# Kernel tuning notes

Measured on AMD Instinct MI355X. Metric: run time of the kernel, lower is better.

Reference implementation:

```python
import jax, jax.numpy as jnp
import numpy as np

H = 128          # num_hidden
B, L, K, M = 4, 2048, 24, 64   # batch, residues, neighbors-per-residue, ligand atoms
FF = 4 * H       # feed-forward width
EPS = 1e-5       # LayerNorm eps (torch default)


def _gelu(x):
    return jax.nn.gelu(x, approximate=False)  # torch nn.GELU default (erf)


def _ln(x, s, b):
    mu = jnp.mean(x, axis=-1, keepdims=True)
    var = jnp.mean(jnp.square(x - mu), axis=-1, keepdims=True)
    return (x - mu) * jax.lax.rsqrt(var + EPS) * s + b


def _lin(x, w, b):
    return x @ w.T + b


def setup_inputs() -> dict:
    key = jax.random.key(0)
    ks = iter(jax.random.split(key, 40))
    # uniqueness makes the reference deterministic and equal to scatter-add.
    nn_idx = jnp.argsort(jax.random.uniform(next(ks), (B, L, M)), axis=-1)[:, :, :K].astype(jnp.int32)
    inp = {
        "nn_idx": nn_idx,
        "Y_scale": jax.random.uniform(next(ks), (B, M), jnp.float32, 1.0, 30.0),
        "h_Y_nodes": jax.random.normal(next(ks), (B, L, K, H), jnp.float32),
        "h_E_context": jax.random.normal(next(ks), (B, L, K, H), jnp.float32),
        "h_V": jax.random.normal(next(ks), (B, L, H), jnp.float32),
    }
    def lin_params(fan_in, fan_out):
        w = jax.random.normal(next(ks), (fan_out, fan_in), jnp.float32) / np.sqrt(fan_in).astype(np.float32)
        b = jnp.zeros((fan_out,), jnp.float32)
        return w, b
    for name, fi, fo in [("W1", 3 * H, H), ("W2", H, H), ("W3", H, H),
                         ("W11", 3 * H, H), ("W12", H, H), ("W13", H, H),
                         ("Win", H, FF), ("Wout", FF, H)]:
        inp[name + "_w"], inp[name + "_b"] = lin_params(fi, fo)
    for name in ("n1", "n2", "n3"):
        inp[name + "_s"] = jnp.ones((H,), jnp.float32)
        inp[name + "_b"] = jnp.zeros((H,), jnp.float32)
    return inp


def reference(nn_idx, Y_scale, h_Y_nodes, h_E_context, h_V,
              W1_w, W1_b, W2_w, W2_b, W3_w, W3_b,
              W11_w, W11_b, W12_w, W12_b, W13_w, W13_b,
              Win_w, Win_b, Wout_w, Wout_b,
              n1_s, n1_b, n2_s, n2_b, n3_s, n3_b):
    h_V_exp = jnp.broadcast_to(h_V[:, :, None, :], (B, L, K, H))
    h_YEV = jnp.concatenate([h_Y_nodes, h_E_context, h_V_exp], axis=-1)  # [B,L,K,3H]
    msg = _lin(_gelu(_lin(_gelu(_lin(h_YEV, W1_w, W1_b)), W2_w, W2_b)), W3_w, W3_b)
    # scatter per (b,l) with unique idx, then sum over l == segment-sum over (b, atom)
    seg_ids = (jnp.arange(B, dtype=jnp.int32)[:, None, None] * M + nn_idx).reshape(-1)
    dh = jax.ops.segment_sum(msg.reshape(-1, H), seg_ids, num_segments=B * M).reshape(B, M, H)
    dh = dh / Y_scale[:, :, None]
    # gather_context_atom_features: dh[b, nn_idx[b,l,k]]
    dh = jnp.take_along_axis(dh, nn_idx.reshape(B, L * K)[:, :, None], axis=1).reshape(B, L, K, H)
    h_Y = _ln(h_Y_nodes + dh, n1_s, n1_b)
    h_Y = _ln(h_Y + _lin(_gelu(_lin(h_Y, Win_w, Win_b)), Wout_w, Wout_b), n2_s, n2_b)
    h_YEV = jnp.concatenate([h_Y, h_E_context, h_V_exp], axis=-1)
    msg = _lin(_gelu(_lin(_gelu(_lin(h_YEV, W11_w, W11_b)), W12_w, W12_b)), W13_w, W13_b)
    h_E = _ln(h_E_context + msg, n3_s, n3_b)
    return (h_Y, h_E)
```

## Files before the change

### kernel.cpp

```cpp
#include <hip/hip_runtime.h>
#include <hip/hip_bf16.h>

#define H_   128
#define B_   4
#define L_   2048
#define KN   24
#define M_   64
#define NROW (B_*L_*KN)
#define LKR  (L_*KN)

typedef float f32x4 __attribute__((ext_vector_type(4)));
typedef short s16x8 __attribute__((ext_vector_type(8)));

#define MFMA16(a,b,c) __builtin_amdgcn_mfma_f32_16x16x32_bf16((a),(b),(c),0,0,0)

static __device__ __forceinline__ unsigned short f2bfu(float x){
    union { __hip_bfloat16 h; unsigned short s; } u; u.h = __float2bfloat16(x); return u.s;
}
static __device__ __forceinline__ float bf2f(unsigned short s){
    union { unsigned short s; __hip_bfloat16 h; } u; u.s = s; return __bfloat162float(u.h);
}
static __device__ __forceinline__ unsigned packbf(float lo, float hi){
    return (unsigned)f2bfu(lo) | ((unsigned)f2bfu(hi) << 16);
}
static __device__ __forceinline__ float gelu_f(float x){
    const float x2 = x*x;
    const float u  = x * fmaf(x2, -0.10294265f, -2.3022083f);
    const float e  = __builtin_amdgcn_exp2f(u);
    return x * __builtin_amdgcn_rcpf(1.0f + e);
}
static __device__ __forceinline__ float wsum(float v){
#pragma unroll
    for (int m = 32; m; m >>= 1) v += __shfl_xor(v, m, 64);
    return v;
}
static __device__ __forceinline__ s16x8 cvt8(float4 p0, float4 p1){
    s16x8 v;
    v[0]=(short)f2bfu(p0.x); v[1]=(short)f2bfu(p0.y); v[2]=(short)f2bfu(p0.z); v[3]=(short)f2bfu(p0.w);
    v[4]=(short)f2bfu(p1.x); v[5]=(short)f2bfu(p1.y); v[6]=(short)f2bfu(p1.z); v[7]=(short)f2bfu(p1.w);
    return v;
}
template<int KW>
static __device__ __forceinline__ s16x8 afrag(const short* xs, int r, int blk){
    return *(const s16x8*)(xs + r*KW + ((blk ^ (r & 7)) << 3));
}
template<int KW>
static __device__ __forceinline__ void bstore(short* xs, int r, int c, unsigned v){
    *(unsigned*)(xs + r*KW + ((((c >> 3) ^ (r & 7))) << 3) + (c & 7)) = v;
}
static __device__ __forceinline__ int fidx(int r, int c){
    return r*128 + ((((c >> 2) ^ (r & 7))) << 2) + (c & 3);
}

template<int KWACT, int NKS>
static __device__ __forceinline__ void mm_sw(const short* act, const short* __restrict__ Wp,
    int ktS, int kt0, int tn0, int lane, f32x4 (&acc)[2][2])
{
    const int cl = lane & 15, rq = lane >> 4;
    const s16x8* W8 = (const s16x8*)Wp;
#pragma unroll
    for (int ks = 0; ks < NKS; ++ks){
        const int blk = (ks << 2) + rq;
        const s16x8 a0 = afrag<KWACT>(act, cl, blk);
        const s16x8 a1 = afrag<KWACT>(act, 16 + cl, blk);
#pragma unroll
        for (int t = 0; t < 2; ++t){
            const s16x8 wf = W8[(size_t)((tn0 + t)*ktS + kt0 + ks)*64 + lane];
            acc[0][t] = MFMA16(wf, a0, acc[0][t]);
            acc[1][t] = MFMA16(wf, a1, acc[1][t]);
        }
    }
}
template<int KWACT, int NKS>
static __device__ __forceinline__ void mm_nat(const short* act, const short* __restrict__ Wp,
    int ktS, int kt0, int tn0, int lane, f32x4 (&acc)[2][2])
{
    const int cl = lane & 15, rq = lane >> 4;
    const s16x8* W8 = (const s16x8*)Wp;
#pragma unroll
    for (int ks = 0; ks < NKS; ++ks){
        const int blk = (ks << 2) + rq;
        const s16x8 a0 = afrag<KWACT>(act, cl, blk);
        const s16x8 a1 = afrag<KWACT>(act, 16 + cl, blk);
#pragma unroll
        for (int t = 0; t < 2; ++t){
            const s16x8 wf = W8[(size_t)((tn0 + t)*ktS + kt0 + ks)*64 + lane];
            acc[0][t] = MFMA16(a0, wf, acc[0][t]);
            acc[1][t] = MFMA16(a1, wf, acc[1][t]);
        }
    }
}

struct PackArgs {
    const float* src[8];
    int K[8];
    int off[8];
};
#define PACK_TOTAL 294912
__global__ void k_pack(PackArgs pa, short* __restrict__ dst){
    const int gid = blockIdx.x*256 + threadIdx.x;
    if (gid >= PACK_TOTAL) return;
    int w = 0;
#pragma unroll
    for (int i = 1; i < 8; ++i) if (gid >= pa.off[i]) w = i;
    const int e = gid - pa.off[w];
    const int K = pa.K[w];
    const int j = e & 7, lane = (e >> 3) & 63, tt = e >> 9;
    const int kt = K >> 5;
    const int tk = tt % kt, tn = tt / kt;
    const int row = tn*16 + (lane & 15);
    const int col = tk*32 + ((lane >> 4) << 3) + j;
    dst[gid] = (short)f2bfu(pa.src[w][(size_t)row*K + col]);
}

__global__ void k_zero(float* __restrict__ dh){
    const int i = blockIdx.x*256 + threadIdx.x;
    if (i < B_*M_*H_) dh[i] = 0.0f;
}
__global__ void k_scale(float* __restrict__ dh, const float* __restrict__ Ys){
    const int i = blockIdx.x*256 + threadIdx.x;
    if (i < B_*M_*H_) dh[i] = dh[i] / Ys[i >> 7];
}

__global__ __launch_bounds__(256) void k_msg(
    const float* __restrict__ hY, const float* __restrict__ hE, const float* __restrict__ hV,
    const int* __restrict__ nn,
    const short* __restrict__ W1p, const float* __restrict__ B1,
    const short* __restrict__ W2p, const float* __restrict__ B2,
    const short* __restrict__ W3p, const float* __restrict__ B3,
    float* __restrict__ dh)
{
    __shared__ short xs[32*384];
    __shared__ short tb1[32*128];
    __shared__ short tb2[32*128];
    const int tid = threadIdx.x, lane = tid & 63, w = tid >> 6;
    const int cl = lane & 15, rq = lane >> 4;
    const int row0 = blockIdx.x * 32, b = row0 / LKR;
    const int tn0 = 2*w;

    for (int c = tid; c < 32*48; c += 256){
        const int rr = c/48, k = (c - rr*48) << 3, g = row0 + rr;
        const float* s = (k < 128) ? hY + (size_t)g*128 + k
                      : (k < 256) ? hE + (size_t)g*128 + (k-128)
                                  : hV + (size_t)(g/KN)*128 + (k-256);
        float4 p0 = ((const float4*)s)[0], p1 = ((const float4*)s)[1];
        *(s16x8*)(xs + rr*384 + ((((k>>3) ^ (rr&7))) << 3)) = cvt8(p0, p1);
    }
    __syncthreads();

    f32x4 acc[2][2];
#pragma unroll
    for (int t = 0; t < 2; ++t)
#pragma unroll
        for (int j = 0; j < 4; ++j){
            const float bv = B1[(tn0+t)*16 + rq*4 + j];
            acc[0][t][j] = bv; acc[1][t][j] = bv;
        }
    mm_sw<384,12>(xs, W1p, 12, 0, tn0, lane, acc);
#pragma unroll
    for (int rt = 0; rt < 2; ++rt)
#pragma unroll
        for (int t = 0; t < 2; ++t){
            const int r = rt*16 + cl, cb = (tn0+t)*16 + rq*4;
            bstore<128>(tb1, r, cb,   packbf(gelu_f(acc[rt][t][0]), gelu_f(acc[rt][t][1])));
            bstore<128>(tb1, r, cb+2, packbf(gelu_f(acc[rt][t][2]), gelu_f(acc[rt][t][3])));
        }
    __syncthreads();

#pragma unroll
    for (int t = 0; t < 2; ++t)
#pragma unroll
        for (int j = 0; j < 4; ++j){
            const float bv = B2[(tn0+t)*16 + rq*4 + j];
            acc[0][t][j] = bv; acc[1][t][j] = bv;
        }
    mm_sw<128,4>(tb1, W2p, 4, 0, tn0, lane, acc);
#pragma unroll
    for (int rt = 0; rt < 2; ++rt)
#pragma unroll
        for (int t = 0; t < 2; ++t){
            const int r = rt*16 + cl, cb = (tn0+t)*16 + rq*4;
            bstore<128>(tb2, r, cb,   packbf(gelu_f(acc[rt][t][0]), gelu_f(acc[rt][t][1])));
            bstore<128>(tb2, r, cb+2, packbf(gelu_f(acc[rt][t][2]), gelu_f(acc[rt][t][3])));
        }
    __syncthreads();

    f32x4 a3[2][2];
#pragma unroll
    for (int t = 0; t < 2; ++t){
        const float bv = B3[(tn0+t)*16 + cl];
        a3[0][t] = (f32x4){bv,bv,bv,bv};
        a3[1][t] = (f32x4){bv,bv,bv,bv};
    }
    mm_nat<128,4>(tb2, W3p, 4, 0, tn0, lane, a3);

#pragma unroll
    for (int rt = 0; rt < 2; ++rt){
        int mj[4];
#pragma unroll
        for (int j = 0; j < 4; ++j) mj[j] = nn[row0 + rt*16 + rq*4 + j];
#pragma unroll
        for (int t = 0; t < 2; ++t){
            const int c = (tn0+t)*16 + cl;
#pragma unroll
            for (int j = 0; j < 4; ++j)
                __hip_atomic_fetch_add(dh + ((size_t)(b*M_ + mj[j]))*128 + c, a3[rt][t][j],
                                       __ATOMIC_RELAXED, __HIP_MEMORY_SCOPE_AGENT);
        }
    }
}

__global__ __launch_bounds__(256) void k_hy(
    const float* __restrict__ hY, const float* __restrict__ dhs, const int* __restrict__ nn,
    const short* __restrict__ Winp, const float* __restrict__ Bin,
    const short* __restrict__ Woutp, const float* __restrict__ Bout,
    const float* __restrict__ n1s, const float* __restrict__ n1b,
    const float* __restrict__ n2s, const float* __restrict__ n2b,
    float* __restrict__ outY)
{
    __shared__ float tf[32*128];
    __shared__ short xb[32*128];
    __shared__ short ffc[32*128];
    const int tid = threadIdx.x, lane = tid & 63, w = tid >> 6;
    const int cl = lane & 15, rq = lane >> 4;
    const int row0 = blockIdx.x * 32, b = row0 / LKR;

    for (int c = tid; c < 32*16; c += 256){
        const int rr = c >> 4, k = (c & 15) << 3, g = row0 + rr;
        const int m = nn[g];
        const float* a = hY  + (size_t)g*128 + k;
        const float* d = dhs + ((size_t)(b*M_ + m))*128 + k;
        float4 a0 = ((const float4*)a)[0], a1 = ((const float4*)a)[1];
        float4 d0 = ((const float4*)d)[0], d1 = ((const float4*)d)[1];
        float4 r0 = {a0.x+d0.x, a0.y+d0.y, a0.z+d0.z, a0.w+d0.w};
        float4 r1 = {a1.x+d1.x, a1.y+d1.y, a1.z+d1.z, a1.w+d1.w};
        const int s = rr & 7, kb = k >> 2;
        *(float4*)&tf[rr*128 + ((kb ^ s) << 2)]     = r0;
        *(float4*)&tf[rr*128 + (((kb+1) ^ s) << 2)] = r1;
    }
    __syncthreads();

#pragma unroll
    for (int i = 0; i < 8; ++i){
        const int r = w*8 + i;
        const float v0 = tf[fidx(r, lane)], v1 = tf[fidx(r, lane+64)];
        const float mu = wsum(v0+v1) * (1.0f/128.0f);
        const float d0 = v0-mu, d1 = v1-mu;
        const float var = wsum(d0*d0 + d1*d1) * (1.0f/128.0f);
        const float rs = rsqrtf(var + 1e-5f);
        const float y0 = d0*rs*n1s[lane]    + n1b[lane];
        const float y1 = d1*rs*n1s[lane+64] + n1b[lane+64];
        const int c1 = lane + 64;
        xb[r*128 + ((((lane>>3) ^ (r&7))) << 3) + (lane&7)] = (short)f2bfu(y0);
        xb[r*128 + ((((c1>>3)   ^ (r&7))) << 3) + (c1&7)]   = (short)f2bfu(y1);
    }
    __syncthreads();

    f32x4 accW[2][2];
#pragma unroll
    for (int t = 0; t < 2; ++t)
#pragma unroll
        for (int j = 0; j < 4; ++j){
            const float bv = Bout[(2*w+t)*16 + rq*4 + j];
            accW[0][t][j] = bv; accW[1][t][j] = bv;
        }

    for (int p = 0; p < 4; ++p){
        f32x4 ai[2][2];
#pragma unroll
        for (int t = 0; t < 2; ++t)
#pragma unroll
            for (int j = 0; j < 4; ++j){
                const float bv = Bin[p*128 + (2*w+t)*16 + rq*4 + j];
                ai[0][t][j] = bv; ai[1][t][j] = bv;
            }
        mm_sw<128,4>(xb, Winp, 4, 0, p*8 + 2*w, lane, ai);
        __syncthreads();
#pragma unroll
        for (int rt = 0; rt < 2; ++rt)
#pragma unroll
            for (int t = 0; t < 2; ++t){
                const int r = rt*16 + cl, cb = (2*w+t)*16 + rq*4;
                bstore<128>(ffc, r, cb,   packbf(gelu_f(ai[rt][t][0]), gelu_f(ai[rt][t][1])));
                bstore<128>(ffc, r, cb+2, packbf(gelu_f(ai[rt][t][2]), gelu_f(ai[rt][t][3])));
            }
        __syncthreads();
        mm_sw<128,4>(ffc, Woutp, 16, p*4, 2*w, lane, accW);
    }

#pragma unroll
    for (int rt = 0; rt < 2; ++rt)
#pragma unroll
        for (int t = 0; t < 2; ++t){
            const int r = rt*16 + cl, cb = (2*w+t)*16 + rq*4;
            float4 o = {accW[rt][t][0], accW[rt][t][1], accW[rt][t][2], accW[rt][t][3]};
            *(float4*)&tf[r*128 + ((((cb>>2) ^ (r&7))) << 2)] = o;
        }
    __syncthreads();

#pragma unroll
    for (int i = 0; i < 8; ++i){
        const int r = w*8 + i, g = row0 + r;
        const int c1 = lane + 64;
        const float x0 = bf2f((unsigned short)xb[r*128 + ((((lane>>3) ^ (r&7))) << 3) + (lane&7)]);
        const float x1 = bf2f((unsigned short)xb[r*128 + ((((c1>>3)   ^ (r&7))) << 3) + (c1&7)]);
        const float v0 = tf[fidx(r, lane)]    + x0;
        const float v1 = tf[fidx(r, lane+64)] + x1;
        const float mu = wsum(v0+v1) * (1.0f/128.0f);
        const float d0 = v0-mu, d1 = v1-mu;
        const float var = wsum(d0*d0 + d1*d1) * (1.0f/128.0f);
        const float rs = rsqrtf(var + 1e-5f);
        outY[(size_t)g*128 + lane]      = d0*rs*n2s[lane]    + n2b[lane];
        outY[(size_t)g*128 + lane + 64] = d1*rs*n2s[lane+64] + n2b[lane+64];
    }
}

__global__ __launch_bounds__(256) void k_he(
    const float* __restrict__ hYn, const float* __restrict__ hE, const float* __restrict__ hV,
    const short* __restrict__ W1p, const float* __restrict__ B1,
    const short* __restrict__ W2p, const float* __restrict__ B2,
    const short* __restrict__ W3p, const float* __restrict__ B3,
    const float* __restrict__ n3s, const float* __restrict__ n3b,
    float* __restrict__ outE)
{
    __shared__ __align__(16) char pool[40960];
    short* xs  = (short*)pool;
    float* tf  = (float*)pool;
    short* tb1 = (short*)(pool + 24576);
    short* tb2 = (short*)(pool + 32768);
    const int tid = threadIdx.x, lane = tid & 63, w = tid >> 6;
    const int cl = lane & 15, rq = lane >> 4;
    const int row0 = blockIdx.x * 32;
    const int tn0 = 2*w;

    for (int c = tid; c < 32*48; c += 256){
        const int rr = c/48, k = (c - rr*48) << 3, g = row0 + rr;
        const float* s = (k < 128) ? hYn + (size_t)g*128 + k
                      : (k < 256) ? hE  + (size_t)g*128 + (k-128)
                                  : hV  + (size_t)(g/KN)*128 + (k-256);
        float4 p0 = ((const float4*)s)[0], p1 = ((const float4*)s)[1];
        *(s16x8*)(xs + rr*384 + ((((k>>3) ^ (rr&7))) << 3)) = cvt8(p0, p1);
    }
    __syncthreads();

    f32x4 acc[2][2];
#pragma unroll
    for (int t = 0; t < 2; ++t)
#pragma unroll
        for (int j = 0; j < 4; ++j){
            const float bv = B1[(tn0+t)*16 + rq*4 + j];
            acc[0][t][j] = bv; acc[1][t][j] = bv;
        }
    mm_sw<384,12>(xs, W1p, 12, 0, tn0, lane, acc);
#pragma unroll
    for (int rt = 0; rt < 2; ++rt)
#pragma unroll
        for (int t = 0; t < 2; ++t){
            const int r = rt*16 + cl, cb = (tn0+t)*16 + rq*4;
            bstore<128>(tb1, r, cb,   packbf(gelu_f(acc[rt][t][0]), gelu_f(acc[rt][t][1])));
            bstore<128>(tb1, r, cb+2, packbf(gelu_f(acc[rt][t][2]), gelu_f(acc[rt][t][3])));
        }
    __syncthreads();

#pragma unroll
    for (int t = 0; t < 2; ++t)
#pragma unroll
        for (int j = 0; j < 4; ++j){
            const float bv = B2[(tn0+t)*16 + rq*4 + j];
            acc[0][t][j] = bv; acc[1][t][j] = bv;
        }
    mm_sw<128,4>(tb1, W2p, 4, 0, tn0, lane, acc);
#pragma unroll
    for (int rt = 0; rt < 2; ++rt)
#pragma unroll
        for (int t = 0; t < 2; ++t){
            const int r = rt*16 + cl, cb = (tn0+t)*16 + rq*4;
            bstore<128>(tb2, r, cb,   packbf(gelu_f(acc[rt][t][0]), gelu_f(acc[rt][t][1])));
            bstore<128>(tb2, r, cb+2, packbf(gelu_f(acc[rt][t][2]), gelu_f(acc[rt][t][3])));
        }
    __syncthreads();

#pragma unroll
    for (int t = 0; t < 2; ++t)
#pragma unroll
        for (int j = 0; j < 4; ++j){
            const float bv = B3[(tn0+t)*16 + rq*4 + j];
            acc[0][t][j] = bv; acc[1][t][j] = bv;
        }
    mm_sw<128,4>(tb2, W3p, 4, 0, tn0, lane, acc);

#pragma unroll
    for (int rt = 0; rt < 2; ++rt)
#pragma unroll
        for (int t = 0; t < 2; ++t){
            const int r = rt*16 + cl, cb = (tn0+t)*16 + rq*4;
            float4 o = {acc[rt][t][0], acc[rt][t][1], acc[rt][t][2], acc[rt][t][3]};
            *(float4*)&tf[r*128 + ((((cb>>2) ^ (r&7))) << 2)] = o;
        }
    __syncthreads();

#pragma unroll
    for (int i = 0; i < 8; ++i){
        const int r = w*8 + i, g = row0 + r;
        const float v0 = tf[fidx(r, lane)]    + hE[(size_t)g*128 + lane];
        const float v1 = tf[fidx(r, lane+64)] + hE[(size_t)g*128 + lane + 64];
        const float mu = wsum(v0+v1) * (1.0f/128.0f);
        const float d0 = v0-mu, d1 = v1-mu;
        const float var = wsum(d0*d0 + d1*d1) * (1.0f/128.0f);
        const float rs = rsqrtf(var + 1e-5f);
        outE[(size_t)g*128 + lane]      = d0*rs*n3s[lane]    + n3b[lane];
        outE[(size_t)g*128 + lane + 64] = d1*rs*n3s[lane+64] + n3b[lane+64];
    }
}

extern "C" void kernel_launch(void* const* d_in, const int* in_sizes, int n_in,
                              void* d_out, int out_size, void* d_ws, size_t ws_size,
                              hipStream_t stream) {
    const int*   nn   = (const int*)  d_in[0];
    const float* Ys   = (const float*)d_in[1];
    const float* hY   = (const float*)d_in[2];
    const float* hE   = (const float*)d_in[3];
    const float* hV   = (const float*)d_in[4];
    const float* W1w  = (const float*)d_in[5];  const float* W1b  = (const float*)d_in[6];
    const float* W2w  = (const float*)d_in[7];  const float* W2b  = (const float*)d_in[8];
    const float* W3w  = (const float*)d_in[9];  const float* W3b  = (const float*)d_in[10];
    const float* W11w = (const float*)d_in[11]; const float* W11b = (const float*)d_in[12];
    const float* W12w = (const float*)d_in[13]; const float* W12b = (const float*)d_in[14];
    const float* W13w = (const float*)d_in[15]; const float* W13b = (const float*)d_in[16];
    const float* Winw = (const float*)d_in[17]; const float* Winb = (const float*)d_in[18];
    const float* Woutw= (const float*)d_in[19]; const float* Woutb= (const float*)d_in[20];
    const float* n1s  = (const float*)d_in[21]; const float* n1b  = (const float*)d_in[22];
    const float* n2s  = (const float*)d_in[23]; const float* n2b  = (const float*)d_in[24];
    const float* n3s  = (const float*)d_in[25]; const float* n3b  = (const float*)d_in[26];

    float* outY = (float*)d_out;
    float* outE = outY + (size_t)NROW * H_;

    float* dh = (float*)d_ws;
    short* wp = (short*)((char*)d_ws + 131072);

    const int oW1 = 0,       oW2 = 49152,   oW3 = 65536,   oW11 = 81920;
    const int oW12 = 131072, oW13 = 147456, oWin = 163840, oWout = 229376;

    PackArgs pa;
    pa.src[0]=W1w;  pa.K[0]=384; pa.off[0]=oW1;
    pa.src[1]=W2w;  pa.K[1]=128; pa.off[1]=oW2;
    pa.src[2]=W3w;  pa.K[2]=128; pa.off[2]=oW3;
    pa.src[3]=W11w; pa.K[3]=384; pa.off[3]=oW11;
    pa.src[4]=W12w; pa.K[4]=128; pa.off[4]=oW12;
    pa.src[5]=W13w; pa.K[5]=128; pa.off[5]=oW13;
    pa.src[6]=Winw; pa.K[6]=128; pa.off[6]=oWin;
    pa.src[7]=Woutw;pa.K[7]=512; pa.off[7]=oWout;

    const int nblk = NROW / 32;

    k_pack <<<(PACK_TOTAL + 255)/256, 256, 0, stream>>>(pa, wp);
    k_zero <<<(B_*M_*H_ + 255)/256, 256, 0, stream>>>(dh);
    k_msg  <<<nblk, 256, 0, stream>>>(hY, hE, hV, nn,
                                      wp + oW1, W1b, wp + oW2, W2b, wp + oW3, W3b, dh);
    k_scale<<<(B_*M_*H_ + 255)/256, 256, 0, stream>>>(dh, Ys);
    k_hy   <<<nblk, 256, 0, stream>>>(hY, dh, nn, wp + oWin, Winb, wp + oWout, Woutb,
                                      n1s, n1b, n2s, n2b, outY);
    k_he   <<<nblk, 256, 0, stream>>>(outY, hE, hV,
                                      wp + oW11, W11b, wp + oW12, W12b, wp + oW13, W13b,
                                      n3s, n3b, outE);
}
```

Baseline: 395.3 us.

## Fuse hY FFN and hE message MLP into one kernel, fold Y_scale division

Merges k_hy and k_he into a single kernel so the LayerNormed h_Y stays in shared memory as bf16 and feeds the W11 MLP directly, with no write and reread through global memory. The per-atom Y_scale division moves into the gather, which removes the k_scale launch. The FFN loop is restructured to handle 256 hidden columns per pass with explicit MFMA loops, and the final message is staged in bf16 instead of fp32. The cost is more shared memory and registers per block, and rounding the final message to bf16 before the residual LayerNorm adds some precision loss.

```diff
diff --git a/kernel.cpp b/kernel.cpp
--- a/kernel.cpp
+++ b/kernel.cpp
@@ -116,10 +116,6 @@
 __global__ void k_zero(float* __restrict__ dh){
     const int i = blockIdx.x*256 + threadIdx.x;
     if (i < B_*M_*H_) dh[i] = 0.0f;
-}
-__global__ void k_scale(float* __restrict__ dh, const float* __restrict__ Ys){
-    const int i = blockIdx.x*256 + threadIdx.x;
-    if (i < B_*M_*H_) dh[i] = dh[i] / Ys[i >> 7];
 }
 
 __global__ __launch_bounds__(256) void k_msg(
@@ -210,40 +206,43 @@
     }
 }
 
-__global__ __launch_bounds__(256) void k_hy(
-    const float* __restrict__ hY, const float* __restrict__ dhs, const int* __restrict__ nn,
+__global__ __launch_bounds__(256) void k_hye(
+    const float* __restrict__ hY, const float* __restrict__ dh, const float* __restrict__ Ys,
+    const int* __restrict__ nn,
+    const float* __restrict__ hE, const float* __restrict__ hV,
     const short* __restrict__ Winp, const float* __restrict__ Bin,
     const short* __restrict__ Woutp, const float* __restrict__ Bout,
+    const short* __restrict__ W11p, const float* __restrict__ B11,
+    const short* __restrict__ W12p, const float* __restrict__ B12,
+    const short* __restrict__ W13p, const float* __restrict__ B13,
     const float* __restrict__ n1s, const float* __restrict__ n1b,
     const float* __restrict__ n2s, const float* __restrict__ n2b,
-    float* __restrict__ outY)
+    const float* __restrict__ n3s, const float* __restrict__ n3b,
+    float* __restrict__ outY, float* __restrict__ outE)
 {
-    __shared__ float tf[32*128];
-    __shared__ short xb[32*128];
-    __shared__ short ffc[32*128];
+    __shared__ __align__(16) char pool[40960];
+    short* xb  = (short*)pool;
+    short* ffc = (short*)(pool + 8192);
+    float* tf  = (float*)(pool + 24576);
+    short* eb  = (short*)(pool + 8192);
+    short* vb  = (short*)(pool + 16384);
+    short* tb1 = (short*)(pool + 24576);
+    short* tb2 = (short*)(pool + 32768);
+
     const int tid = threadIdx.x, lane = tid & 63, w = tid >> 6;
     const int cl = lane & 15, rq = lane >> 4;
     const int row0 = blockIdx.x * 32, b = row0 / LKR;
-
-    for (int c = tid; c < 32*16; c += 256){
-        const int rr = c >> 4, k = (c & 15) << 3, g = row0 + rr;
+    const s16x8* Wi8 = (const s16x8*)Winp;
+    const s16x8* Wo8 = (const s16x8*)Woutp;
+
+#pragma unroll
+    for (int i = 0; i < 8; ++i){
+        const int r = w*8 + i, g = row0 + r;
         const int m = nn[g];
-        const float* a = hY  + (size_t)g*128 + k;
-        const float* d = dhs + ((size_t)(b*M_ + m))*128 + k;
-        float4 a0 = ((const float4*)a)[0], a1 = ((const float4*)a)[1];
-        float4 d0 = ((const float4*)d)[0], d1 = ((const float4*)d)[1];
-        float4 r0 = {a0.x+d0.x, a0.y+d0.y, a0.z+d0.z, a0.w+d0.w};
-        float4 r1 = {a1.x+d1.x, a1.y+d1.y, a1.z+d1.z, a1.w+d1.w};
-        const int s = rr & 7, kb = k >> 2;
-        *(float4*)&tf[rr*128 + ((kb ^ s) << 2)]     = r0;
-        *(float4*)&tf[rr*128 + (((kb+1) ^ s) << 2)] = r1;
-    }
-    __syncthreads();
-
-#pragma unroll
-    for (int i = 0; i < 8; ++i){
-        const int r = w*8 + i;
-        const float v0 = tf[fidx(r, lane)], v1 = tf[fidx(r, lane+64)];
+        const float inv = 1.0f / Ys[b*M_ + m];
+        const float* dr = dh + ((size_t)(b*M_ + m))*128;
+        const float v0 = hY[(size_t)g*128 + lane]      + dr[lane]      * inv;
+        const float v1 = hY[(size_t)g*128 + lane + 64] + dr[lane + 64] * inv;
         const float mu = wsum(v0+v1) * (1.0f/128.0f);
         const float d0 = v0-mu, d1 = v1-mu;
         const float var = wsum(d0*d0 + d1*d1) * (1.0f/128.0f);
@@ -265,27 +264,49 @@
             accW[0][t][j] = bv; accW[1][t][j] = bv;
         }
 
-    for (int p = 0; p < 4; ++p){
-        f32x4 ai[2][2];
-#pragma unroll
-        for (int t = 0; t < 2; ++t)
+    for (int p = 0; p < 2; ++p){
+        f32x4 ai[4][2];
+#pragma unroll
+        for (int t = 0; t < 4; ++t)
 #pragma unroll
             for (int j = 0; j < 4; ++j){
-                const float bv = Bin[p*128 + (2*w+t)*16 + rq*4 + j];
-                ai[0][t][j] = bv; ai[1][t][j] = bv;
+                const float bv = Bin[p*256 + (w*4+t)*16 + rq*4 + j];
+                ai[t][0][j] = bv; ai[t][1][j] = bv;
             }
-        mm_sw<128,4>(xb, Winp, 4, 0, p*8 + 2*w, lane, ai);
+#pragma unroll
+        for (int ks = 0; ks < 4; ++ks){
+            const int blk = (ks << 2) + rq;
+            const s16x8 a0 = afrag<128>(xb, cl, blk);
+            const s16x8 a1 = afrag<128>(xb, 16 + cl, blk);
+#pragma unroll
+            for (int t = 0; t < 4; ++t){
+                const s16x8 wf = Wi8[(size_t)((p*16 + w*4 + t)*4 + ks)*64 + lane];
+                ai[t][0] = MFMA16(wf, a0, ai[t][0]);
+                ai[t][1] = MFMA16(wf, a1, ai[t][1]);
+            }
+        }
         __syncthreads();
 #pragma unroll
         for (int rt = 0; rt < 2; ++rt)
 #pragma unroll
-            for (int t = 0; t < 2; ++t){
-                const int r = rt*16 + cl, cb = (2*w+t)*16 + rq*4;
-                bstore<128>(ffc, r, cb,   packbf(gelu_f(ai[rt][t][0]), gelu_f(ai[rt][t][1])));
-                bstore<128>(ffc, r, cb+2, packbf(gelu_f(ai[rt][t][2]), gelu_f(ai[rt][t][3])));
+            for (int t = 0; t < 4; ++t){
+                const int r = rt*16 + cl, cb = (w*4+t)*16 + rq*4;
+                bstore<256>(ffc, r, cb,   packbf(gelu_f(ai[t][rt][0]), gelu_f(ai[t][rt][1])));
+                bstore<256>(ffc, r, cb+2, packbf(gelu_f(ai[t][rt][2]), gelu_f(ai[t][rt][3])));
             }
         __syncthreads();
-        mm_sw<128,4>(ffc, Woutp, 16, p*4, 2*w, lane, accW);
+#pragma unroll
+        for (int ks = 0; ks < 8; ++ks){
+            const int blk = (ks << 2) + rq;
+            const s16x8 a0 = afrag<256>(ffc, cl, blk);
+            const s16x8 a1 = afrag<256>(ffc, 16 + cl, blk);
+#pragma unroll
+            for (int t = 0; t < 2; ++t){
+                const s16x8 wf = Wo8[(size_t)((2*w+t)*16 + p*8 + ks)*64 + lane];
+                accW[0][t] = MFMA16(wf, a0, accW[0][t]);
+                accW[1][t] = MFMA16(wf, a1, accW[1][t]);
+            }
+        }
     }
 
 #pragma unroll
@@ -302,56 +323,62 @@
     for (int i = 0; i < 8; ++i){
         const int r = w*8 + i, g = row0 + r;
         const int c1 = lane + 64;
-        const float x0 = bf2f((unsigned short)xb[r*128 + ((((lane>>3) ^ (r&7))) << 3) + (lane&7)]);
-        const float x1 = bf2f((unsigned short)xb[r*128 + ((((c1>>3)   ^ (r&7))) << 3) + (c1&7)]);
+        const int s0 = r*128 + ((((lane>>3) ^ (r&7))) << 3) + (lane&7);
+        const int s1 = r*128 + ((((c1>>3)   ^ (r&7))) << 3) + (c1&7);
+        const float x0 = bf2f((unsigned short)xb[s0]);
+        const float x1 = bf2f((unsigned short)xb[s1]);
         const float v0 = tf[fidx(r, lane)]    + x0;
         const float v1 = tf[fidx(r, lane+64)] + x1;
         const float mu = wsum(v0+v1) * (1.0f/128.0f);
         const float d0 = v0-mu, d1 = v1-mu;
         const float var = wsum(d0*d0 + d1*d1) * (1.0f/128.0f);
         const float rs = rsqrtf(var + 1e-5f);
-        outY[(size_t)g*128 + lane]      = d0*rs*n2s[lane]    + n2b[lane];
-        outY[(size_t)g*128 + lane + 64] = d1*rs*n2s[lane+64] + n2b[lane+64];
-    }
-}
-
-__global__ __launch_bounds__(256) void k_he(
-    const float* __restrict__ hYn, const float* __restrict__ hE, const float* __restrict__ hV,
-    const short* __restrict__ W1p, const float* __restrict__ B1,
-    const short* __restrict__ W2p, const float* __restrict__ B2,
-    const short* __restrict__ W3p, const float* __restrict__ B3,
-    const float* __restrict__ n3s, const float* __restrict__ n3b,
-    float* __restrict__ outE)
-{
-    __shared__ __align__(16) char pool[40960];
-    short* xs  = (short*)pool;
-    float* tf  = (float*)pool;
-    short* tb1 = (short*)(pool + 24576);
-    short* tb2 = (short*)(pool + 32768);
-    const int tid = threadIdx.x, lane = tid & 63, w = tid >> 6;
-    const int cl = lane & 15, rq = lane >> 4;
-    const int row0 = blockIdx.x * 32;
+        const float h0 = d0*rs*n2s[lane]    + n2b[lane];
+        const float h1 = d1*rs*n2s[lane+64] + n2b[lane+64];
+        outY[(size_t)g*128 + lane]      = h0;
+        outY[(size_t)g*128 + lane + 64] = h1;
+        xb[s0] = (short)f2bfu(h0);
+        xb[s1] = (short)f2bfu(h1);
+    }
+    __syncthreads();
+
+    for (int c = tid; c < 32*32; c += 256){
+        const int half = c >> 9;
+        const int cc = c & 511;
+        const int rr = cc >> 4, k = (cc & 15) << 3, g = row0 + rr;
+        const float* s = half ? hV + (size_t)(g/KN)*128 + k
+                              : hE + (size_t)g*128 + k;
+        float4 p0 = ((const float4*)s)[0], p1 = ((const float4*)s)[1];
+        short* dstb = half ? vb : eb;
+        *(s16x8*)(dstb + rr*128 + ((((k>>3) ^ (rr&7))) << 3)) = cvt8(p0, p1);
+    }
+    __syncthreads();
+
     const int tn0 = 2*w;
-
-    for (int c = tid; c < 32*48; c += 256){
-        const int rr = c/48, k = (c - rr*48) << 3, g = row0 + rr;
-        const float* s = (k < 128) ? hYn + (size_t)g*128 + k
-                      : (k < 256) ? hE  + (size_t)g*128 + (k-128)
-                                  : hV  + (size_t)(g/KN)*128 + (k-256);
-        float4 p0 = ((const float4*)s)[0], p1 = ((const float4*)s)[1];
-        *(s16x8*)(xs + rr*384 + ((((k>>3) ^ (rr&7))) << 3)) = cvt8(p0, p1);
-    }
-    __syncthreads();
-
     f32x4 acc[2][2];
 #pragma unroll
     for (int t = 0; t < 2; ++t)
 #pragma unroll
         for (int j = 0; j < 4; ++j){
-            const float bv = B1[(tn0+t)*16 + rq*4 + j];
+            const float bv = B11[(tn0+t)*16 + rq*4 + j];
             acc[0][t][j] = bv; acc[1][t][j] = bv;
         }
-    mm_sw<384,12>(xs, W1p, 12, 0, tn0, lane, acc);
+    {
+        const s16x8* W8 = (const s16x8*)W11p;
+#pragma unroll
+        for (int ks = 0; ks < 12; ++ks){
+            const short* buf = (ks < 4) ? xb : (ks < 8) ? eb : vb;
+            const int blk = ((ks & 3) << 2) + rq;
+            const s16x8 a0 = afrag<128>(buf, cl, blk);
+            const s16x8 a1 = afrag<128>(buf, 16 + cl, blk);
+#pragma unroll
+            for (int t = 0; t < 2; ++t){
+                const s16x8 wf = W8[(size_t)((tn0 + t)*12 + ks)*64 + lane];
+                acc[0][t] = MFMA16(wf, a0, acc[0][t]);
+                acc[1][t] = MFMA16(wf, a1, acc[1][t]);
+            }
+        }
+    }
 #pragma unroll
     for (int rt = 0; rt < 2; ++rt)
 #pragma unroll
@@ -366,10 +393,10 @@
     for (int t = 0; t < 2; ++t)
 #pragma unroll
         for (int j = 0; j < 4; ++j){
-            const float bv = B2[(tn0+t)*16 + rq*4 + j];
+            const float bv = B12[(tn0+t)*16 + rq*4 + j];
             acc[0][t][j] = bv; acc[1][t][j] = bv;
         }
-    mm_sw<128,4>(tb1, W2p, 4, 0, tn0, lane, acc);
+    mm_sw<128,4>(tb1, W12p, 4, 0, tn0, lane, acc);
 #pragma unroll
     for (int rt = 0; rt < 2; ++rt)
 #pragma unroll
@@ -384,26 +411,28 @@
     for (int t = 0; t < 2; ++t)
 #pragma unroll
         for (int j = 0; j < 4; ++j){
-            const float bv = B3[(tn0+t)*16 + rq*4 + j];
+            const float bv = B13[(tn0+t)*16 + rq*4 + j];
             acc[0][t][j] = bv; acc[1][t][j] = bv;
         }
-    mm_sw<128,4>(tb2, W3p, 4, 0, tn0, lane, acc);
-
+    mm_sw<128,4>(tb2, W13p, 4, 0, tn0, lane, acc);
 #pragma unroll
     for (int rt = 0; rt < 2; ++rt)
 #pragma unroll
         for (int t = 0; t < 2; ++t){
             const int r = rt*16 + cl, cb = (tn0+t)*16 + rq*4;
-            float4 o = {acc[rt][t][0], acc[rt][t][1], acc[rt][t][2], acc[rt][t][3]};
-            *(float4*)&tf[r*128 + ((((cb>>2) ^ (r&7))) << 2)] = o;
+            bstore<128>(tb1, r, cb,   packbf(acc[rt][t][0], acc[rt][t][1]));
+            bstore<128>(tb1, r, cb+2, packbf(acc[rt][t][2], acc[rt][t][3]));
         }
     __syncthreads();
 
 #pragma unroll
     for (int i = 0; i < 8; ++i){
         const int r = w*8 + i, g = row0 + r;
-        const float v0 = tf[fidx(r, lane)]    + hE[(size_t)g*128 + lane];
-        const float v1 = tf[fidx(r, lane+64)] + hE[(size_t)g*128 + lane + 64];
+        const int c1 = lane + 64;
+        const float m0 = bf2f((unsigned short)tb1[r*128 + ((((lane>>3) ^ (r&7))) << 3) + (lane&7)]);
+        const float m1 = bf2f((unsigned short)tb1[r*128 + ((((c1>>3)   ^ (r&7))) << 3) + (c1&7)]);
+        const float v0 = m0 + hE[(size_t)g*128 + lane];
+        const float v1 = m1 + hE[(size_t)g*128 + lane + 64];
         const float mu = wsum(v0+v1) * (1.0f/128.0f);
         const float d0 = v0-mu, d1 = v1-mu;
         const float var = wsum(d0*d0 + d1*d1) * (1.0f/128.0f);
@@ -458,10 +487,8 @@
     k_zero <<<(B_*M_*H_ + 255)/256, 256, 0, stream>>>(dh);
     k_msg  <<<nblk, 256, 0, stream>>>(hY, hE, hV, nn,
                                       wp + oW1, W1b, wp + oW2, W2b, wp + oW3, W3b, dh);
-    k_scale<<<(B_*M_*H_ + 255)/256, 256, 0, stream>>>(dh, Ys);
-    k_hy   <<<nblk, 256, 0, stream>>>(hY, dh, nn, wp + oWin, Winb, wp + oWout, Woutb,
-                                      n1s, n1b, n2s, n2b, outY);
-    k_he   <<<nblk, 256, 0, stream>>>(outY, hE, hV,
+    k_hye  <<<nblk, 256, 0, stream>>>(hY, dh, Ys, nn, hE, hV,
+                                      wp + oWin, Winb, wp + oWout, Woutb,
                                       wp + oW11, W11b, wp + oW12, W12b, wp + oW13, W13b,
-                                      n3s, n3b, outE);
-}
+                                      n1s, n1b, n2s, n2b, n3s, n3b, outY, outE);
+}
```

After: 599.5 us. 1.52x slower.

## Use 64-row tiles with 8 waves each owning one 16-column slab across rows

Applied to the files above, without the earlier changes.

All three fused kernels move from 32-row/256-thread blocks to 64-row/512-thread blocks. Each wave now owns a single 16-wide output column tile and sweeps four row fragments, so every weight fragment loaded from global memory is reused four times instead of twice. Shared buffers are aliased inside one pool, and the separate dh scaling kernel is folded into k_hy as a reciprocal-multiply on the gather. k_he also stores its final MLP output to shared memory as bf16 instead of fp32. The trade-offs are more LDS per block, which may lower occupancy, and a small extra rounding of the pre-LayerNorm message.

```diff
diff --git a/kernel.cpp b/kernel.cpp
--- a/kernel.cpp
+++ b/kernel.cpp
@@ -50,45 +50,6 @@
 }
 static __device__ __forceinline__ int fidx(int r, int c){
     return r*128 + ((((c >> 2) ^ (r & 7))) << 2) + (c & 3);
-}
-
-template<int KWACT, int NKS>
-static __device__ __forceinline__ void mm_sw(const short* act, const short* __restrict__ Wp,
-    int ktS, int kt0, int tn0, int lane, f32x4 (&acc)[2][2])
-{
-    const int cl = lane & 15, rq = lane >> 4;
-    const s16x8* W8 = (const s16x8*)Wp;
-#pragma unroll
-    for (int ks = 0; ks < NKS; ++ks){
-        const int blk = (ks << 2) + rq;
-        const s16x8 a0 = afrag<KWACT>(act, cl, blk);
-        const s16x8 a1 = afrag<KWACT>(act, 16 + cl, blk);
-#pragma unroll
-        for (int t = 0; t < 2; ++t){
-            const s16x8 wf = W8[(size_t)((tn0 + t)*ktS + kt0 + ks)*64 + lane];
-            acc[0][t] = MFMA16(wf, a0, acc[0][t]);
-            acc[1][t] = MFMA16(wf, a1, acc[1][t]);
-        }
-    }
-}
-template<int KWACT, int NKS>
-static __device__ __forceinline__ void mm_nat(const short* act, const short* __restrict__ Wp,
-    int ktS, int kt0, int tn0, int lane, f32x4 (&acc)[2][2])
-{
-    const int cl = lane & 15, rq = lane >> 4;
-    const s16x8* W8 = (const s16x8*)Wp;
-#pragma unroll
-    for (int ks = 0; ks < NKS; ++ks){
-        const int blk = (ks << 2) + rq;
-        const s16x8 a0 = afrag<KWACT>(act, cl, blk);
-        const s16x8 a1 = afrag<KWACT>(act, 16 + cl, blk);
-#pragma unroll
-        for (int t = 0; t < 2; ++t){
-            const s16x8 wf = W8[(size_t)((tn0 + t)*ktS + kt0 + ks)*64 + lane];
-            acc[0][t] = MFMA16(a0, wf, acc[0][t]);
-            acc[1][t] = MFMA16(a1, wf, acc[1][t]);
-        }
-    }
 }
 
 struct PackArgs {
@@ -117,12 +78,8 @@
     const int i = blockIdx.x*256 + threadIdx.x;
     if (i < B_*M_*H_) dh[i] = 0.0f;
 }
-__global__ void k_scale(float* __restrict__ dh, const float* __restrict__ Ys){
-    const int i = blockIdx.x*256 + threadIdx.x;
-    if (i < B_*M_*H_) dh[i] = dh[i] / Ys[i >> 7];
-}
-
-__global__ __launch_bounds__(256) void k_msg(
+
+__global__ __launch_bounds__(512, 4) void k_msg(
     const float* __restrict__ hY, const float* __restrict__ hE, const float* __restrict__ hV,
     const int* __restrict__ nn,
     const short* __restrict__ W1p, const float* __restrict__ B1,
@@ -130,15 +87,15 @@
     const short* __restrict__ W3p, const float* __restrict__ B3,
     float* __restrict__ dh)
 {
-    __shared__ short xs[32*384];
-    __shared__ short tb1[32*128];
-    __shared__ short tb2[32*128];
+    __shared__ __align__(16) char pool[65536];
+    short* xs  = (short*)pool;
+    short* tb2 = (short*)pool;
+    short* tb1 = (short*)(pool + 49152);
     const int tid = threadIdx.x, lane = tid & 63, w = tid >> 6;
     const int cl = lane & 15, rq = lane >> 4;
-    const int row0 = blockIdx.x * 32, b = row0 / LKR;
-    const int tn0 = 2*w;
-
-    for (int c = tid; c < 32*48; c += 256){
+    const int row0 = blockIdx.x * 64, b = row0 / LKR;
+
+    for (int c = tid; c < 64*48; c += 512){
         const int rr = c/48, k = (c - rr*48) << 3, g = row0 + rr;
         const float* s = (k < 128) ? hY + (size_t)g*128 + k
                       : (k < 256) ? hE + (size_t)g*128 + (k-128)
@@ -148,92 +105,117 @@
     }
     __syncthreads();
 
-    f32x4 acc[2][2];
-#pragma unroll
-    for (int t = 0; t < 2; ++t)
-#pragma unroll
-        for (int j = 0; j < 4; ++j){
-            const float bv = B1[(tn0+t)*16 + rq*4 + j];
-            acc[0][t][j] = bv; acc[1][t][j] = bv;
-        }
-    mm_sw<384,12>(xs, W1p, 12, 0, tn0, lane, acc);
-#pragma unroll
-    for (int rt = 0; rt < 2; ++rt)
-#pragma unroll
-        for (int t = 0; t < 2; ++t){
-            const int r = rt*16 + cl, cb = (tn0+t)*16 + rq*4;
-            bstore<128>(tb1, r, cb,   packbf(gelu_f(acc[rt][t][0]), gelu_f(acc[rt][t][1])));
-            bstore<128>(tb1, r, cb+2, packbf(gelu_f(acc[rt][t][2]), gelu_f(acc[rt][t][3])));
-        }
-    __syncthreads();
-
-#pragma unroll
-    for (int t = 0; t < 2; ++t)
-#pragma unroll
-        for (int j = 0; j < 4; ++j){
-            const float bv = B2[(tn0+t)*16 + rq*4 + j];
-            acc[0][t][j] = bv; acc[1][t][j] = bv;
-        }
-    mm_sw<128,4>(tb1, W2p, 4, 0, tn0, lane, acc);
-#pragma unroll
-    for (int rt = 0; rt < 2; ++rt)
-#pragma unroll
-        for (int t = 0; t < 2; ++t){
-            const int r = rt*16 + cl, cb = (tn0+t)*16 + rq*4;
-            bstore<128>(tb2, r, cb,   packbf(gelu_f(acc[rt][t][0]), gelu_f(acc[rt][t][1])));
-            bstore<128>(tb2, r, cb+2, packbf(gelu_f(acc[rt][t][2]), gelu_f(acc[rt][t][3])));
-        }
-    __syncthreads();
-
-    f32x4 a3[2][2];
-#pragma unroll
-    for (int t = 0; t < 2; ++t){
-        const float bv = B3[(tn0+t)*16 + cl];
-        a3[0][t] = (f32x4){bv,bv,bv,bv};
-        a3[1][t] = (f32x4){bv,bv,bv,bv};
-    }
-    mm_nat<128,4>(tb2, W3p, 4, 0, tn0, lane, a3);
-
-#pragma unroll
-    for (int rt = 0; rt < 2; ++rt){
+    f32x4 acc[4];
+#pragma unroll
+    for (int rf = 0; rf < 4; ++rf)
+#pragma unroll
+        for (int j = 0; j < 4; ++j) acc[rf][j] = B1[w*16 + rq*4 + j];
+    {
+        const s16x8* W8 = (const s16x8*)W1p;
+#pragma unroll
+        for (int ks = 0; ks < 12; ++ks){
+            const s16x8 wf = W8[(size_t)(w*12 + ks)*64 + lane];
+            const int blk = ks*4 + rq;
+#pragma unroll
+            for (int rf = 0; rf < 4; ++rf){
+                const s16x8 a = afrag<384>(xs, rf*16 + cl, blk);
+                acc[rf] = MFMA16(wf, a, acc[rf]);
+            }
+        }
+    }
+#pragma unroll
+    for (int rf = 0; rf < 4; ++rf){
+        const int r = rf*16 + cl, cb = w*16 + rq*4;
+        bstore<128>(tb1, r, cb,   packbf(gelu_f(acc[rf][0]), gelu_f(acc[rf][1])));
+        bstore<128>(tb1, r, cb+2, packbf(gelu_f(acc[rf][2]), gelu_f(acc[rf][3])));
+    }
+    __syncthreads();
+
+#pragma unroll
+    for (int rf = 0; rf < 4; ++rf)
+#pragma unroll
+        for (int j = 0; j < 4; ++j) acc[rf][j] = B2[w*16 + rq*4 + j];
+    {
+        const s16x8* W8 = (const s16x8*)W2p;
+#pragma unroll
+        for (int ks = 0; ks < 4; ++ks){
+            const s16x8 wf = W8[(size_t)(w*4 + ks)*64 + lane];
+            const int blk = ks*4 + rq;
+#pragma unroll
+            for (int rf = 0; rf < 4; ++rf){
+                const s16x8 a = afrag<128>(tb1, rf*16 + cl, blk);
+                acc[rf] = MFMA16(wf, a, acc[rf]);
+            }
+        }
+    }
+#pragma unroll
+    for (int rf = 0; rf < 4; ++rf){
+        const int r = rf*16 + cl, cb = w*16 + rq*4;
+        bstore<128>(tb2, r, cb,   packbf(gelu_f(acc[rf][0]), gelu_f(acc[rf][1])));
+        bstore<128>(tb2, r, cb+2, packbf(gelu_f(acc[rf][2]), gelu_f(acc[rf][3])));
+    }
+    __syncthreads();
+
+#pragma unroll
+    for (int rf = 0; rf < 4; ++rf){
+        const float bv = B3[w*16 + cl];
+        acc[rf] = (f32x4){bv,bv,bv,bv};
+    }
+    {
+        const s16x8* W8 = (const s16x8*)W3p;
+#pragma unroll
+        for (int ks = 0; ks < 4; ++ks){
+            const s16x8 wf = W8[(size_t)(w*4 + ks)*64 + lane];
+            const int blk = ks*4 + rq;
+#pragma unroll
+            for (int rf = 0; rf < 4; ++rf){
+                const s16x8 a = afrag<128>(tb2, rf*16 + cl, blk);
+                acc[rf] = MFMA16(a, wf, acc[rf]);
+            }
+        }
+    }
+#pragma unroll
+    for (int rf = 0; rf < 4; ++rf){
         int mj[4];
 #pragma unroll
-        for (int j = 0; j < 4; ++j) mj[j] = nn[row0 + rt*16 + rq*4 + j];
-#pragma unroll
-        for (int t = 0; t < 2; ++t){
-            const int c = (tn0+t)*16 + cl;
-#pragma unroll
-            for (int j = 0; j < 4; ++j)
-                __hip_atomic_fetch_add(dh + ((size_t)(b*M_ + mj[j]))*128 + c, a3[rt][t][j],
-                                       __ATOMIC_RELAXED, __HIP_MEMORY_SCOPE_AGENT);
-        }
-    }
-}
-
-__global__ __launch_bounds__(256) void k_hy(
-    const float* __restrict__ hY, const float* __restrict__ dhs, const int* __restrict__ nn,
+        for (int j = 0; j < 4; ++j) mj[j] = nn[row0 + rf*16 + rq*4 + j];
+        const int c = w*16 + cl;
+#pragma unroll
+        for (int j = 0; j < 4; ++j)
+            __hip_atomic_fetch_add(dh + ((size_t)(b*M_ + mj[j]))*128 + c, acc[rf][j],
+                                   __ATOMIC_RELAXED, __HIP_MEMORY_SCOPE_AGENT);
+    }
+}
+
+__global__ __launch_bounds__(512, 4) void k_hy(
+    const float* __restrict__ hY, const float* __restrict__ dh, const float* __restrict__ Ys,
+    const int* __restrict__ nn,
     const short* __restrict__ Winp, const float* __restrict__ Bin,
     const short* __restrict__ Woutp, const float* __restrict__ Bout,
     const float* __restrict__ n1s, const float* __restrict__ n1b,
     const float* __restrict__ n2s, const float* __restrict__ n2b,
     float* __restrict__ outY)
 {
-    __shared__ float tf[32*128];
-    __shared__ short xb[32*128];
-    __shared__ short ffc[32*128];
+    __shared__ __align__(16) char pool[49152];
+    short* xb  = (short*)pool;
+    short* ffc = (short*)(pool + 16384);
+    float* tf  = (float*)(pool + 16384);
     const int tid = threadIdx.x, lane = tid & 63, w = tid >> 6;
     const int cl = lane & 15, rq = lane >> 4;
-    const int row0 = blockIdx.x * 32, b = row0 / LKR;
-
-    for (int c = tid; c < 32*16; c += 256){
+    const int row0 = blockIdx.x * 64, b = row0 / LKR;
+    const s16x8* Wi8 = (const s16x8*)Winp;
+    const s16x8* Wo8 = (const s16x8*)Woutp;
+
+    for (int c = tid; c < 64*16; c += 512){
         const int rr = c >> 4, k = (c & 15) << 3, g = row0 + rr;
         const int m = nn[g];
-        const float* a = hY  + (size_t)g*128 + k;
-        const float* d = dhs + ((size_t)(b*M_ + m))*128 + k;
+        const float inv = 1.0f / Ys[b*M_ + m];
+        const float* a = hY + (size_t)g*128 + k;
+        const float* d = dh + ((size_t)(b*M_ + m))*128 + k;
         float4 a0 = ((const float4*)a)[0], a1 = ((const float4*)a)[1];
         float4 d0 = ((const float4*)d)[0], d1 = ((const float4*)d)[1];
-        float4 r0 = {a0.x+d0.x, a0.y+d0.y, a0.z+d0.z, a0.w+d0.w};
-        float4 r1 = {a1.x+d1.x, a1.y+d1.y, a1.z+d1.z, a1.w+d1.w};
+        float4 r0 = {fmaf(d0.x,inv,a0.x), fmaf(d0.y,inv,a0.y), fmaf(d0.z,inv,a0.z), fmaf(d0.w,inv,a0.w)};
+        float4 r1 = {fmaf(d1.x,inv,a1.x), fmaf(d1.y,inv,a1.y), fmaf(d1.z,inv,a1.z), fmaf(d1.w,inv,a1.w)};
         const int s = rr & 7, kb = k >> 2;
         *(float4*)&tf[rr*128 + ((kb ^ s) << 2)]     = r0;
         *(float4*)&tf[rr*128 + (((kb+1) ^ s) << 2)] = r1;
@@ -256,46 +238,55 @@
     }
     __syncthreads();
 
-    f32x4 accW[2][2];
-#pragma unroll
-    for (int t = 0; t < 2; ++t)
-#pragma unroll
-        for (int j = 0; j < 4; ++j){
-            const float bv = Bout[(2*w+t)*16 + rq*4 + j];
-            accW[0][t][j] = bv; accW[1][t][j] = bv;
-        }
+    f32x4 accW[4];
+#pragma unroll
+    for (int rf = 0; rf < 4; ++rf)
+#pragma unroll
+        for (int j = 0; j < 4; ++j) accW[rf][j] = Bout[w*16 + rq*4 + j];
 
     for (int p = 0; p < 4; ++p){
-        f32x4 ai[2][2];
-#pragma unroll
-        for (int t = 0; t < 2; ++t)
-#pragma unroll
-            for (int j = 0; j < 4; ++j){
-                const float bv = Bin[p*128 + (2*w+t)*16 + rq*4 + j];
-                ai[0][t][j] = bv; ai[1][t][j] = bv;
-            }
-        mm_sw<128,4>(xb, Winp, 4, 0, p*8 + 2*w, lane, ai);
+        f32x4 ai[4];
+#pragma unroll
+        for (int rf = 0; rf < 4; ++rf)
+#pragma unroll
+            for (int j = 0; j < 4; ++j) ai[rf][j] = Bin[p*128 + w*16 + rq*4 + j];
+#pragma unroll
+        for (int ks = 0; ks < 4; ++ks){
+            const s16x8 wf = Wi8[(size_t)((p*8 + w)*4 + ks)*64 + lane];
+            const int blk = ks*4 + rq;
+#pragma unroll
+            for (int rf = 0; rf < 4; ++rf){
+                const s16x8 a = afrag<128>(xb, rf*16 + cl, blk);
+                ai[rf] = MFMA16(wf, a, ai[rf]);
+            }
+        }
         __syncthreads();
 #pragma unroll
-        for (int rt = 0; rt < 2; ++rt)
-#pragma unroll
-            for (int t = 0; t < 2; ++t){
-                const int r = rt*16 + cl, cb = (2*w+t)*16 + rq*4;
-                bstore<128>(ffc, r, cb,   packbf(gelu_f(ai[rt][t][0]), gelu_f(ai[rt][t][1])));
-                bstore<128>(ffc, r, cb+2, packbf(gelu_f(ai[rt][t][2]), gelu_f(ai[rt][t][3])));
-            }
+        for (int rf = 0; rf < 4; ++rf){
+            const int r = rf*16 + cl, cb = w*16 + rq*4;
+            bstore<128>(ffc, r, cb,   packbf(gelu_f(ai[rf][0]), gelu_f(ai[rf][1])));
+            bstore<128>(ffc, r, cb+2, packbf(gelu_f(ai[rf][2]), gelu_f(ai[rf][3])));
+        }
         __syncthreads();
-        mm_sw<128,4>(ffc, Woutp, 16, p*4, 2*w, lane, accW);
-    }
-
-#pragma unroll
-    for (int rt = 0; rt < 2; ++rt)
-#pragma unroll
-        for (int t = 0; t < 2; ++t){
-            const int r = rt*16 + cl, cb = (2*w+t)*16 + rq*4;
-            float4 o = {accW[rt][t][0], accW[rt][t][1], accW[rt][t][2], accW[rt][t][3]};
-            *(float4*)&tf[r*128 + ((((cb>>2) ^ (r&7))) << 2)] = o;
-        }
+#pragma unroll
+        for (int ks = 0; ks < 4; ++ks){
+            const s16x8 wf = Wo8[(size_t)(w*16 + p*4 + ks)*64 + lane];
+            const int blk = ks*4 + rq;
+#pragma unroll
+            for (int rf = 0; rf < 4; ++rf){
+                const s16x8 a = afrag<128>(ffc, rf*16 + cl, blk);
+                accW[rf] = MFMA16(wf, a, accW[rf]);
+            }
+        }
+    }
+    __syncthreads();
+
+#pragma unroll
+    for (int rf = 0; rf < 4; ++rf){
+        const int r = rf*16 + cl, cb = w*16 + rq*4;
+        float4 o = {accW[rf][0], accW[rf][1], accW[rf][2], accW[rf][3]};
+        *(float4*)&tf[r*128 + ((((cb>>2) ^ (r&7))) << 2)] = o;
+    }
     __syncthreads();
 
 #pragma unroll
@@ -315,7 +306,7 @@
     }
 }
 
-__global__ __launch_bounds__(256) void k_he(
+__global__ __launch_bounds__(512, 4) void k_he(
     const float* __restrict__ hYn, const float* __restrict__ hE, const float* __restrict__ hV,
     const short* __restrict__ W1p, const float* __restrict__ B1,
     const short* __restrict__ W2p, const float* __restrict__ B2,
@@ -323,17 +314,15 @@
     const float* __restrict__ n3s, const float* __restrict__ n3b,
     float* __restrict__ outE)
 {
-    __shared__ __align__(16) char pool[40960];
+    __shared__ __align__(16) char pool[65536];
     short* xs  = (short*)pool;
-    float* tf  = (float*)pool;
-    short* tb1 = (short*)(pool + 24576);
-    short* tb2 = (short*)(pool + 32768);
+    short* tb2 = (short*)pool;
+    short* tb1 = (short*)(pool + 49152);
     const int tid = threadIdx.x, lane = tid & 63, w = tid >> 6;
     const int cl = lane & 15, rq = lane >> 4;
-    const int row0 = blockIdx.x * 32;
-    const int tn0 = 2*w;
-
-    for (int c = tid; c < 32*48; c += 256){
+    const int row0 = blockIdx.x * 64;
+
+    for (int c = tid; c < 64*48; c += 512){
         const int rr = c/48, k = (c - rr*48) << 3, g = row0 + rr;
         const float* s = (k < 128) ? hYn + (size_t)g*128 + k
                       : (k < 256) ? hE  + (size_t)g*128 + (k-128)
@@ -343,67 +332,90 @@
     }
     __syncthreads();
 
-    f32x4 acc[2][2];
-#pragma unroll
-    for (int t = 0; t < 2; ++t)
-#pragma unroll
-        for (int j = 0; j < 4; ++j){
-            const float bv = B1[(tn0+t)*16 + rq*4 + j];
-            acc[0][t][j] = bv; acc[1][t][j] = bv;
-        }
-    mm_sw<384,12>(xs, W1p, 12, 0, tn0, lane, acc);
-#pragma unroll
-    for (int rt = 0; rt < 2; ++rt)
-#pragma unroll
-        for (int t = 0; t < 2; ++t){
-            const int r = rt*16 + cl, cb = (tn0+t)*16 + rq*4;
-            bstore<128>(tb1, r, cb,   packbf(gelu_f(acc[rt][t][0]), gelu_f(acc[rt][t][1])));
-            bstore<128>(tb1, r, cb+2, packbf(gelu_f(acc[rt][t][2]), gelu_f(acc[rt][t][3])));
-        }
-    __syncthreads();
-
-#pragma unroll
-    for (int t = 0; t < 2; ++t)
-#pragma unroll
-        for (int j = 0; j < 4; ++j){
-            const float bv = B2[(tn0+t)*16 + rq*4 + j];
-            acc[0][t][j] = bv; acc[1][t][j] = bv;
-        }
-    mm_sw<128,4>(tb1, W2p, 4, 0, tn0, lane, acc);
-#pragma unroll
-    for (int rt = 0; rt < 2; ++rt)
-#pragma unroll
-        for (int t = 0; t < 2; ++t){
-            const int r = rt*16 + cl, cb = (tn0+t)*16 + rq*4;
-            bstore<128>(tb2, r, cb,   packbf(gelu_f(acc[rt][t][0]), gelu_f(acc[rt][t][1])));
-            bstore<128>(tb2, r, cb+2, packbf(gelu_f(acc[rt][t][2]), gelu_f(acc[rt][t][3])));
-        }
-    __syncthreads();
-
-#pragma unroll
-    for (int t = 0; t < 2; ++t)
-#pragma unroll
-        for (int j = 0; j < 4; ++j){
-            const float bv = B3[(tn0+t)*16 + rq*4 + j];
-            acc[0][t][j] = bv; acc[1][t][j] = bv;
-        }
-    mm_sw<128,4>(tb2, W3p, 4, 0, tn0, lane, acc);
-
-#pragma unroll
-    for (int rt = 0; rt < 2; ++rt)
-#pragma unroll
-        for (int t = 0; t < 2; ++t){
-            const int r = rt*16 + cl, cb = (tn0+t)*16 + rq*4;
-            float4 o = {acc[rt][t][0], acc[rt][t][1], acc[rt][t][2], acc[rt][t][3]};
-            *(float4*)&tf[r*128 + ((((cb>>2) ^ (r&7))) << 2)] = o;
-        }
+    f32x4 acc[4];
+#pragma unroll
+    for (int rf = 0; rf < 4; ++rf)
+#pragma unroll
+        for (int j = 0; j < 4; ++j) acc[rf][j] = B1[w*16 + rq*4 + j];
+    {
+        const s16x8* W8 = (const s16x8*)W1p;
+#pragma unroll
+        for (int ks = 0; ks < 12; ++ks){
+            const s16x8 wf = W8[(size_t)(w*12 + ks)*64 + lane];
+            const int blk = ks*4 + rq;
+#pragma unroll
+            for (int rf = 0; rf < 4; ++rf){
+                const s16x8 a = afrag<384>(xs, rf*16 + cl, blk);
+                acc[rf] = MFMA16(wf, a, acc[rf]);
+            }
+        }
+    }
+#pragma unroll
+    for (int rf = 0; rf < 4; ++rf){
+        const int r = rf*16 + cl, cb = w*16 + rq*4;
+        bstore<128>(tb1, r, cb,   packbf(gelu_f(acc[rf][0]), gelu_f(acc[rf][1])));
+        bstore<128>(tb1, r, cb+2, packbf(gelu_f(acc[rf][2]), gelu_f(acc[rf][3])));
+    }
+    __syncthreads();
+
+#pragma unroll
+    for (int rf = 0; rf < 4; ++rf)
+#pragma unroll
+        for (int j = 0; j < 4; ++j) acc[rf][j] = B2[w*16 + rq*4 + j];
+    {
+        const s16x8* W8 = (const s16x8*)W2p;
+#pragma unroll
+        for (int ks = 0; ks < 4; ++ks){
+            const s16x8 wf = W8[(size_t)(w*4 + ks)*64 + lane];
+            const int blk = ks*4 + rq;
+#pragma unroll
+            for (int rf = 0; rf < 4; ++rf){
+                const s16x8 a = afrag<128>(tb1, rf*16 + cl, blk);
+                acc[rf] = MFMA16(wf, a, acc[rf]);
+            }
+        }
+    }
+#pragma unroll
+    for (int rf = 0; rf < 4; ++rf){
+        const int r = rf*16 + cl, cb = w*16 + rq*4;
+        bstore<128>(tb2, r, cb,   packbf(gelu_f(acc[rf][0]), gelu_f(acc[rf][1])));
+        bstore<128>(tb2, r, cb+2, packbf(gelu_f(acc[rf][2]), gelu_f(acc[rf][3])));
+    }
+    __syncthreads();
+
+#pragma unroll
+    for (int rf = 0; rf < 4; ++rf)
+#pragma unroll
+        for (int j = 0; j < 4; ++j) acc[rf][j] = B3[w*16 + rq*4 + j];
+    {
+        const s16x8* W8 = (const s16x8*)W3p;
+#pragma unroll
+        for (int ks = 0; ks < 4; ++ks){
+            const s16x8 wf = W8[(size_t)(w*4 + ks)*64 + lane];
+            const int blk = ks*4 + rq;
+#pragma unroll
+            for (int rf = 0; rf < 4; ++rf){
+                const s16x8 a = afrag<128>(tb2, rf*16 + cl, blk);
+                acc[rf] = MFMA16(wf, a, acc[rf]);
+            }
+        }
+    }
+#pragma unroll
+    for (int rf = 0; rf < 4; ++rf){
+        const int r = rf*16 + cl, cb = w*16 + rq*4;
+        bstore<128>(tb1, r, cb,   packbf(acc[rf][0], acc[rf][1]));
+        bstore<128>(tb1, r, cb+2, packbf(acc[rf][2], acc[rf][3]));
+    }
     __syncthreads();
 
 #pragma unroll
     for (int i = 0; i < 8; ++i){
         const int r = w*8 + i, g = row0 + r;
-        const float v0 = tf[fidx(r, lane)]    + hE[(size_t)g*128 + lane];
-        const float v1 = tf[fidx(r, lane+64)] + hE[(size_t)g*128 + lane + 64];
+        const int c1 = lane + 64;
+        const float m0 = bf2f((unsigned short)tb1[r*128 + ((((lane>>3) ^ (r&7))) << 3) + (lane&7)]);
+        const float m1 = bf2f((unsigned short)tb1[r*128 + ((((c1>>3)   ^ (r&7))) << 3) + (c1&7)]);
+        const float v0 = m0 + hE[(size_t)g*128 + lane];
+        const float v1 = m1 + hE[(size_t)g*128 + lane + 64];
         const float mu = wsum(v0+v1) * (1.0f/128.0f);
         const float d0 = v0-mu, d1 = v1-mu;
         const float var = wsum(d0*d0 + d1*d1) * (1.0f/128.0f);
@@ -452,16 +464,15 @@
     pa.src[6]=Winw; pa.K[6]=128; pa.off[6]=oWin;
     pa.src[7]=Woutw;pa.K[7]=512; pa.off[7]=oWout;
 
-    const int nblk = NROW / 32;
+    const int nblk = NROW / 64;
 
     k_pack <<<(PACK_TOTAL + 255)/256, 256, 0, stream>>>(pa, wp);
     k_zero <<<(B_*M_*H_ + 255)/256, 256, 0, stream>>>(dh);
-    k_msg  <<<nblk, 256, 0, stream>>>(hY, hE, hV, nn,
+    k_msg  <<<nblk, 512, 0, stream>>>(hY, hE, hV, nn,
                                       wp + oW1, W1b, wp + oW2, W2b, wp + oW3, W3b, dh);
-    k_scale<<<(B_*M_*H_ + 255)/256, 256, 0, stream>>>(dh, Ys);
-    k_hy   <<<nblk, 256, 0, stream>>>(hY, dh, nn, wp + oWin, Winb, wp + oWout, Woutb,
+    k_hy   <<<nblk, 512, 0, stream>>>(hY, dh, Ys, nn, wp + oWin, Winb, wp + oWout, Woutb,
                                       n1s, n1b, n2s, n2b, outY);
-    k_he   <<<nblk, 256, 0, stream>>>(outY, hE, hV,
+    k_he   <<<nblk, 512, 0, stream>>>(outY, hE, hV,
                                       wp + oW11, W11b, wp + oW12, W12b, wp + oW13, W13b,
                                       n3s, n3b, outE);
 }
```

Result: faster. 374.4 us (-5.3%).
